# Kernel tuning notes

Measured on AMD Instinct MI355X. Metric: run time of the kernel, lower is better.

The kernel has to match this reference:

```python
import jax, jax.numpy as jnp
import numpy as np

ALPHA = 1.0
BLOCK = 128  # row block size for the pairwise L1 reduction


def _pairwise_score(features, a):
    # score[i, j] = sum_k |f[i,k] - f[j,k]| * a[k]
    # computed in row blocks to avoid the O(n^2*d) broadcast intermediate
    n, d = features.shape
    av = a[:, 0]  # [d]
    fb = features.reshape(n // BLOCK, BLOCK, d)

    def blk(fblk):  # fblk: [B, d]
        diff = jnp.abs(fblk[:, None, :] - features[None, :, :])  # [B, n, d]
        return jnp.einsum('bnd,d->bn', diff, av)                  # [B, n]

    return jax.lax.map(blk, fb).reshape(n, n)


def setup_inputs() -> dict:
    key = jax.random.key(0)
    n, d = 8192, 256
    features = jax.random.normal(key, (n, d), dtype=jnp.float32)
    a = jnp.full((d, 1), 0.01, dtype=jnp.float32)  # nn.init.constant_(a, 0.01)
    return {"features": features, "a": a}


def reference(features, a):
    score = _pairwise_score(features, a)                 # [n, n]
    adjacency = jnp.exp(-ALPHA * jax.nn.relu(score))     # [n, n]
    # D^{-1/2} A D^{-1/2} via row/col elementwise scaling (== diag mm mm)
    dsq = jnp.sum(adjacency, axis=1) ** -0.5             # [n]
    normalized = dsq[:, None] * adjacency * dsq[None, :]
    return (normalized, adjacency)
```

## Files before the change

### kernel.cpp

```cpp
#include <hip/hip_runtime.h>
#include <math.h>

#define BM 128
#define BN 128
#define BK 32

typedef unsigned int uint;

__device__ __forceinline__ uint fenc(float f) {
    uint u = __float_as_uint(f);
    return (u & 0x80000000u) ? ~u : (u | 0x80000000u);
}
__device__ __forceinline__ float fdec(uint u) {
    uint v = (u & 0x80000000u) ? (u & 0x7FFFFFFFu) : ~u;
    return __uint_as_float(v);
}

__global__ __launch_bounds__(256) void init_kernel(uint* __restrict__ flags,
                                                   float* __restrict__ rowsum,
                                                   const float* __restrict__ A,
                                                   int n, int d, int zb)
{
    const int b = blockIdx.x, t = threadIdx.x;
    if (b < zb) { int i = b * 256 + t; if (i < n) rowsum[i] = 0.f; return; }
    if (t == 0) { flags[0] = 0u; flags[1] = 0xFFFFFFFFu; flags[2] = 0u; }
    __syncthreads();
    for (int k = t; k < d; k += 256)
        if (A[k] < 0.f) atomicOr(&flags[0], 1u);
}

__global__ __launch_bounds__(256) void minmax_kernel(const float* __restrict__ F,
                                                     const float* __restrict__ A,
                                                     uint* __restrict__ flags,
                                                     int n, int d)
{
    const int total4 = n * d / 4;
    float lmin = 3.4e38f, lmax = -3.4e38f;
    for (int e4 = blockIdx.x * 256 + threadIdx.x; e4 < total4; e4 += gridDim.x * 256) {
        int e = e4 * 4;
        int dk = e % d;
        float4 f = *(const float4*)(F + e);
        float4 a = *(const float4*)(A + dk);
        float g0 = fabsf(a.x) * f.x, g1 = fabsf(a.y) * f.y;
        float g2 = fabsf(a.z) * f.z, g3 = fabsf(a.w) * f.w;
        lmin = fminf(lmin, fminf(fminf(g0, g1), fminf(g2, g3)));
        lmax = fmaxf(lmax, fmaxf(fmaxf(g0, g1), fmaxf(g2, g3)));
    }
    #pragma unroll
    for (int m = 1; m < 64; m <<= 1) {
        lmin = fminf(lmin, __shfl_xor(lmin, m));
        lmax = fmaxf(lmax, __shfl_xor(lmax, m));
    }
    if ((threadIdx.x & 63) == 0) {
        atomicMin(&flags[1], fenc(lmin));
        atomicMax(&flags[2], fenc(lmax));
    }
}

__global__ __launch_bounds__(256) void quant_kernel(const float* __restrict__ F,
                                                    const float* __restrict__ A,
                                                    const uint* __restrict__ flags,
                                                    uint* __restrict__ Q,
                                                    int n, int d)
{
    const int t = threadIdx.x;
    const int r = blockIdx.x * 32 + (t & 31);
    const int kqb = t >> 5;
    const int d4 = d >> 2;
    const float gmin = fdec(flags[1]), gmax = fdec(flags[2]);
    const float span = gmax - gmin;
    const float inv = span > 0.f ? 255.f / span : 0.f;
    for (int kq = kqb; kq < d4; kq += 8) {
        float4 f = *(const float4*)(F + (size_t)r * d + kq * 4);
        float4 a = *(const float4*)(A + kq * 4);
        uint q0 = 0, q1 = 0, q2 = 0, q3 = 0;
        if (a.x > 0.f) q0 = (uint)fminf(fmaxf((a.x * f.x - gmin) * inv + 0.5f, 0.f), 255.f);
        if (a.y > 0.f) q1 = (uint)fminf(fmaxf((a.y * f.y - gmin) * inv + 0.5f, 0.f), 255.f);
        if (a.z > 0.f) q2 = (uint)fminf(fmaxf((a.z * f.z - gmin) * inv + 0.5f, 0.f), 255.f);
        if (a.w > 0.f) q3 = (uint)fminf(fmaxf((a.w * f.w - gmin) * inv + 0.5f, 0.f), 255.f);
        Q[(size_t)kq * n + r] = q0 | (q1 << 8) | (q2 << 16) | (q3 << 24);
    }
}

__global__ __launch_bounds__(256, 3) void adj_sad_kernel(const uint* __restrict__ Q,
                                                         const uint* __restrict__ flags,
                                                         float* __restrict__ adj,
                                                         float* __restrict__ rowsum,
                                                         int n, int d)
{
    if (flags[0] != 0u) return;

    __shared__ uint As[16][128];
    __shared__ uint Bs[16][128];

    int b = blockIdx.x;
    int bx = (int)((sqrtf(8.f * (float)b + 1.f) - 1.f) * 0.5f);
    while ((bx + 1) * (bx + 2) / 2 <= b) ++bx;
    while (bx * (bx + 1) / 2 > b) --bx;
    const int by = b - bx * (bx + 1) / 2;

    const int t = threadIdx.x, tx = t & 15, ty = t >> 4;
    const int i0 = by * 128;
    const int j0 = bx * 128;
    const bool diag = (bx == by);
    const int d4 = d >> 2, chunks = d4 >> 4;

    const float gmin = fdec(flags[1]), gmax = fdec(flags[2]);
    const float step = (gmax - gmin) * (1.f / 255.f);

    uint acc[8][8] = {};

    const int kk0 = t >> 5;
    const int col = 4 * (t & 31);

    uint4 sa[2], sb[2];
    #pragma unroll
    for (int j = 0; j < 2; ++j) {
        size_t g = ((size_t)(kk0 + 8 * j)) * n;
        sa[j] = *(const uint4*)(Q + g + i0 + col);
        sb[j] = *(const uint4*)(Q + g + j0 + col);
    }

    for (int c = 0; c < chunks; ++c) {
        ((uint4*)&As[0][0])[t]       = sa[0];
        ((uint4*)&As[0][0])[256 + t] = sa[1];
        ((uint4*)&Bs[0][0])[t]       = sb[0];
        ((uint4*)&Bs[0][0])[256 + t] = sb[1];
        __syncthreads();

        if (c + 1 < chunks) {
            #pragma unroll
            for (int j = 0; j < 2; ++j) {
                size_t g = ((size_t)((c + 1) * 16 + kk0 + 8 * j)) * n;
                sa[j] = *(const uint4*)(Q + g + i0 + col);
                sb[j] = *(const uint4*)(Q + g + j0 + col);
            }
        }

        #pragma unroll
        for (int kk = 0; kk < 16; ++kk) {
            uint ar[8], br[8];
            *(uint4*)&ar[0] = *(const uint4*)&As[kk][4 * ty];
            *(uint4*)&ar[4] = *(const uint4*)&As[kk][64 + 4 * ty];
            *(uint4*)&br[0] = *(const uint4*)&Bs[kk][4 * tx];
            *(uint4*)&br[4] = *(const uint4*)&Bs[kk][64 + 4 * tx];
            #pragma unroll
            for (int m = 0; m < 8; ++m)
                #pragma unroll
                for (int cc = 0; cc < 8; ++cc)
                    acc[m][cc] = __builtin_amdgcn_sad_u8(ar[m], br[cc], acc[m][cc]);
        }
        __syncthreads();
    }

    float e[8][8];
    #pragma unroll
    for (int m = 0; m < 8; ++m)
        #pragma unroll
        for (int cc = 0; cc < 8; ++cc)
            e[m][cc] = __expf(-step * (float)acc[m][cc]);

    #pragma unroll
    for (int m = 0; m < 8; ++m) {
        const int row = i0 + (m >> 2) * 64 + 4 * ty + (m & 3);
        float rs = 0.f;
        #pragma unroll
        for (int qh = 0; qh < 2; ++qh) {
            float4 v = make_float4(e[m][qh * 4 + 0], e[m][qh * 4 + 1],
                                   e[m][qh * 4 + 2], e[m][qh * 4 + 3]);
            rs += (v.x + v.y) + (v.z + v.w);
            *(float4*)(adj + (size_t)row * n + j0 + qh * 64 + 4 * tx) = v;
        }
        rs += __shfl_xor(rs, 1);
        rs += __shfl_xor(rs, 2);
        rs += __shfl_xor(rs, 4);
        rs += __shfl_xor(rs, 8);
        if (tx == 0) atomicAdd(rowsum + row, rs);
    }

    if (!diag) {
        #pragma unroll
        for (int h = 0; h < 2; ++h)
            #pragma unroll
            for (int qh = 0; qh < 2; ++qh)
                #pragma unroll
                for (int cc = 0; cc < 4; ++cc) {
                    float4 v = make_float4(e[4 * h + 0][qh * 4 + cc],
                                           e[4 * h + 1][qh * 4 + cc],
                                           e[4 * h + 2][qh * 4 + cc],
                                           e[4 * h + 3][qh * 4 + cc]);
                    const int r = j0 + qh * 64 + 4 * tx + cc;
                    *(float4*)(adj + (size_t)r * n + i0 + 64 * h + 4 * ty) = v;
                }

        float cs[8];
        #pragma unroll
        for (int cc = 0; cc < 8; ++cc) {
            float s = 0.f;
            #pragma unroll
            for (int m = 0; m < 8; ++m) s += e[m][cc];
            s += __shfl_xor(s, 16);
            s += __shfl_xor(s, 32);
            cs[cc] = s;
        }
        if ((t & 48) == 0) {
            #pragma unroll
            for (int qh = 0; qh < 2; ++qh)
                #pragma unroll
                for (int cc = 0; cc < 4; ++cc)
                    atomicAdd(rowsum + j0 + qh * 64 + 4 * tx + cc, cs[qh * 4 + cc]);
        }
    }
}

__global__ __launch_bounds__(256) void adj_kernel(
    const float* __restrict__ F, const float* __restrict__ A,
    const uint* __restrict__ flags,
    float* __restrict__ adj, float* __restrict__ rowsum, int n, int d)
{
    if (flags[0] == 0u) return;

    __shared__ __align__(16) float As[BK][BM + 4];
    __shared__ __align__(16) float Bs[BK][BN + 4];
    __shared__ float aw[256];

    const int t  = threadIdx.x;
    const int tx = t & 15;
    const int ty = t >> 4;
    const int i0 = blockIdx.y * BM;
    const int j0 = blockIdx.x * BN;

    for (int k = t; k < d; k += 256) aw[k] = A[k];

    float acc[2][2][4][4] = {};

    const int lr = t >> 3;
    const int lk = (t & 7) << 2;

    for (int kc = 0; kc < d; kc += BK) {
        __syncthreads();
        #pragma unroll
        for (int s = 0; s < 4; ++s) {
            int r = lr + 32 * s;
            float4 v = *(const float4*)(F + (size_t)(i0 + r) * d + kc + lk);
            As[lk + 0][r] = v.x; As[lk + 1][r] = v.y;
            As[lk + 2][r] = v.z; As[lk + 3][r] = v.w;
            float4 u = *(const float4*)(F + (size_t)(j0 + r) * d + kc + lk);
            Bs[lk + 0][r] = u.x; Bs[lk + 1][r] = u.y;
            Bs[lk + 2][r] = u.z; Bs[lk + 3][r] = u.w;
        }
        __syncthreads();

        #pragma unroll
        for (int k = 0; k < BK; ++k) {
            float av[2][4], bv[2][4];
            *(float4*)&av[0][0] = *(const float4*)&As[k][4 * ty];
            *(float4*)&av[1][0] = *(const float4*)&As[k][64 + 4 * ty];
            *(float4*)&bv[0][0] = *(const float4*)&Bs[k][4 * tx];
            *(float4*)&bv[1][0] = *(const float4*)&Bs[k][64 + 4 * tx];
            const float w = aw[kc + k];
            #pragma unroll
            for (int p = 0; p < 2; ++p)
                #pragma unroll
                for (int m = 0; m < 4; ++m)
                    #pragma unroll
                    for (int q = 0; q < 2; ++q)
                        #pragma unroll
                        for (int c = 0; c < 4; ++c)
                            acc[p][q][m][c] += fabsf(av[p][m] - bv[q][c]) * w;
        }
    }

    #pragma unroll
    for (int p = 0; p < 2; ++p) {
        #pragma unroll
        for (int m = 0; m < 4; ++m) {
            const int row = i0 + p * 64 + ty * 4 + m;
            float rs = 0.f;
            #pragma unroll
            for (int q = 0; q < 2; ++q) {
                float4 v;
                v.x = __expf(-fmaxf(acc[p][q][m][0], 0.f));
                v.y = __expf(-fmaxf(acc[p][q][m][1], 0.f));
                v.z = __expf(-fmaxf(acc[p][q][m][2], 0.f));
                v.w = __expf(-fmaxf(acc[p][q][m][3], 0.f));
                rs += (v.x + v.y) + (v.z + v.w);
                *(float4*)(adj + (size_t)row * n + j0 + q * 64 + tx * 4) = v;
            }
            rs += __shfl_xor(rs, 1);
            rs += __shfl_xor(rs, 2);
            rs += __shfl_xor(rs, 4);
            rs += __shfl_xor(rs, 8);
            if (tx == 0) atomicAdd(rowsum + row, rs);
        }
    }
}

__global__ __launch_bounds__(256) void dsq_kernel(
    const float* __restrict__ rowsum, float* __restrict__ dsq, int n)
{
    int i = blockIdx.x * 256 + threadIdx.x;
    if (i < n) dsq[i] = 1.f / sqrtf(rowsum[i]);
}

__global__ __launch_bounds__(256) void norm_kernel(
    const float* __restrict__ adj, const float* __restrict__ dsq,
    float* __restrict__ out, int n)
{
    const int i = blockIdx.y;
    const float di = dsq[i];
    const int base = blockIdx.x * 4096;
    #pragma unroll
    for (int k = 0; k < 4; ++k) {
        const int j = base + k * 1024 + threadIdx.x * 4;
        if (j >= n) return;
        float4 a = *(const float4*)(adj + (size_t)i * n + j);
        float4 dj = *(const float4*)(dsq + j);
        float4 o;
        o.x = di * a.x * dj.x;
        o.y = di * a.y * dj.y;
        o.z = di * a.z * dj.z;
        o.w = di * a.w * dj.w;
        *(float4*)(out + (size_t)i * n + j) = o;
    }
}

extern "C" void kernel_launch(void* const* d_in, const int* in_sizes, int n_in,
                              void* d_out, int out_size, void* d_ws, size_t ws_size,
                              hipStream_t stream)
{
    const float* F = (const float*)d_in[0];
    const float* A = (const float*)d_in[1];
    const int d = in_sizes[1];
    const int n = in_sizes[0] / d;

    float* out    = (float*)d_out;
    float* adj    = out + (size_t)n * n;
    uint*  flags  = (uint*)d_ws;
    float* rowsum = (float*)d_ws + 8;
    float* dsq    = rowsum + n;
    uint* Q = (uint*)d_out;

    const int zb = (n + 255) / 256;
    init_kernel<<<dim3(zb + 1), dim3(256), 0, stream>>>(flags, rowsum, A, n, d, zb);
    minmax_kernel<<<dim3(256), dim3(256), 0, stream>>>(F, A, flags, n, d);
    quant_kernel<<<dim3(n / 32), dim3(256), 0, stream>>>(F, A, flags, Q, n, d);

    const int nb = n / 128;
    const int tri = nb * (nb + 1) / 2;
    adj_sad_kernel<<<dim3(tri), dim3(256), 0, stream>>>(Q, flags, adj, rowsum, n, d);
    adj_kernel<<<dim3(nb, nb), dim3(256), 0, stream>>>(F, A, flags, adj, rowsum, n, d);

    dsq_kernel<<<dim3((n + 255) / 256), dim3(256), 0, stream>>>(rowsum, dsq, n);

    dim3 gridN((n + 4095) / 4096, n);
    norm_kernel<<<gridN, dim3(256), 0, stream>>>(adj, dsq, out, n);
}
```

Before: 323.6 us.

## Recompute SAD tile in second pass to fuse normalization and skip adj reload

When the workspace can hold the quantized features, the first SAD pass only accumulates row sums and skips writing the adjacency. A second SAD pass then recomputes the tile and writes both adjacency and the normalized output directly, using nontemporal stores. This removes the full n×n adjacency write-then-read round trip of the separate normalization kernel. The cost is a second pass of SAD compute. The fp32 fallback and norm kernels become grid-stride loops with fixed grid sizes.

Measured after the change: 341.4 us. 1.06x slower.

```diff
diff --git a/kernel.cpp b/kernel.cpp
--- a/kernel.cpp
+++ b/kernel.cpp
@@ -1,11 +1,8 @@
 #include <hip/hip_runtime.h>
 #include <math.h>
 
-#define BM 128
-#define BN 128
-#define BK 32
-
 typedef unsigned int uint;
+typedef float f32x4 __attribute__((ext_vector_type(4)));
 
 __device__ __forceinline__ uint fenc(float f) {
     uint u = __float_as_uint(f);
@@ -14,6 +11,11 @@
 __device__ __forceinline__ float fdec(uint u) {
     uint v = (u & 0x80000000u) ? (u & 0x7FFFFFFFu) : ~u;
     return __uint_as_float(v);
+}
+
+__device__ __forceinline__ void ntst(float* p, float a, float b, float c, float d) {
+    f32x4 t; t.x = a; t.y = b; t.z = c; t.w = d;
+    __builtin_nontemporal_store(t, (f32x4*)p);
 }
 
 __global__ __launch_bounds__(256) void init_kernel(uint* __restrict__ flags,
@@ -82,34 +84,12 @@
     }
 }
 
-__global__ __launch_bounds__(256, 3) void adj_sad_kernel(const uint* __restrict__ Q,
-                                                         const uint* __restrict__ flags,
-                                                         float* __restrict__ adj,
-                                                         float* __restrict__ rowsum,
-                                                         int n, int d)
-{
-    if (flags[0] != 0u) return;
-
-    __shared__ uint As[16][128];
-    __shared__ uint Bs[16][128];
-
-    int b = blockIdx.x;
-    int bx = (int)((sqrtf(8.f * (float)b + 1.f) - 1.f) * 0.5f);
-    while ((bx + 1) * (bx + 2) / 2 <= b) ++bx;
-    while (bx * (bx + 1) / 2 > b) --bx;
-    const int by = b - bx * (bx + 1) / 2;
-
-    const int t = threadIdx.x, tx = t & 15, ty = t >> 4;
-    const int i0 = by * 128;
-    const int j0 = bx * 128;
-    const bool diag = (bx == by);
-    const int d4 = d >> 2, chunks = d4 >> 4;
-
-    const float gmin = fdec(flags[1]), gmax = fdec(flags[2]);
-    const float step = (gmax - gmin) * (1.f / 255.f);
-
-    uint acc[8][8] = {};
-
+__device__ __forceinline__ void sad_core(const uint* __restrict__ Q, int n, int chunks,
+                                         int i0, int j0, int t,
+                                         uint (&acc)[8][8],
+                                         uint (&As)[16][128], uint (&Bs)[16][128])
+{
+    const int tx = t & 15, ty = t >> 4;
     const int kk0 = t >> 5;
     const int col = 4 * (t & 31);
 
@@ -152,13 +132,42 @@
         }
         __syncthreads();
     }
-
-    float e[8][8];
+}
+
+__device__ __forceinline__ void tri_decode(int b, int& bx, int& by) {
+    bx = (int)((sqrtf(8.f * (float)b + 1.f) - 1.f) * 0.5f);
+    while ((bx + 1) * (bx + 2) / 2 <= b) ++bx;
+    while (bx * (bx + 1) / 2 > b) --bx;
+    by = b - bx * (bx + 1) / 2;
+}
+
+__global__ __launch_bounds__(256, 3) void pass1_sad(const uint* __restrict__ Q,
+                                                    const uint* __restrict__ flags,
+                                                    float* __restrict__ adj,
+                                                    float* __restrict__ rowsum,
+                                                    int n, int d, int writeAdj)
+{
+    if (flags[0] != 0u) return;
+
+    __shared__ uint As[16][128];
+    __shared__ uint Bs[16][128];
+
+    int bx, by; tri_decode(blockIdx.x, bx, by);
+    const int t = threadIdx.x, tx = t & 15, ty = t >> 4;
+    const int i0 = by * 128, j0 = bx * 128;
+    const bool diag = (bx == by);
+
+    const float gmin = fdec(flags[1]), gmax = fdec(flags[2]);
+    const float step = (gmax - gmin) * (1.f / 255.f);
+
+    uint acc[8][8] = {};
+    sad_core(Q, n, (d >> 2) >> 4, i0, j0, t, acc, As, Bs);
+
     #pragma unroll
     for (int m = 0; m < 8; ++m)
         #pragma unroll
         for (int cc = 0; cc < 8; ++cc)
-            e[m][cc] = __expf(-step * (float)acc[m][cc]);
+            acc[m][cc] = __float_as_uint(__expf(-step * (float)acc[m][cc]));
 
     #pragma unroll
     for (int m = 0; m < 8; ++m) {
@@ -166,10 +175,13 @@
         float rs = 0.f;
         #pragma unroll
         for (int qh = 0; qh < 2; ++qh) {
-            float4 v = make_float4(e[m][qh * 4 + 0], e[m][qh * 4 + 1],
-                                   e[m][qh * 4 + 2], e[m][qh * 4 + 3]);
+            float4 v = make_float4(__uint_as_float(acc[m][qh * 4 + 0]),
+                                   __uint_as_float(acc[m][qh * 4 + 1]),
+                                   __uint_as_float(acc[m][qh * 4 + 2]),
+                                   __uint_as_float(acc[m][qh * 4 + 3]));
             rs += (v.x + v.y) + (v.z + v.w);
-            *(float4*)(adj + (size_t)row * n + j0 + qh * 64 + 4 * tx) = v;
+            if (writeAdj)
+                *(float4*)(adj + (size_t)row * n + j0 + qh * 64 + 4 * tx) = v;
         }
         rs += __shfl_xor(rs, 1);
         rs += __shfl_xor(rs, 2);
@@ -179,26 +191,27 @@
     }
 
     if (!diag) {
-        #pragma unroll
-        for (int h = 0; h < 2; ++h)
-            #pragma unroll
-            for (int qh = 0; qh < 2; ++qh)
-                #pragma unroll
-                for (int cc = 0; cc < 4; ++cc) {
-                    float4 v = make_float4(e[4 * h + 0][qh * 4 + cc],
-                                           e[4 * h + 1][qh * 4 + cc],
-                                           e[4 * h + 2][qh * 4 + cc],
-                                           e[4 * h + 3][qh * 4 + cc]);
-                    const int r = j0 + qh * 64 + 4 * tx + cc;
-                    *(float4*)(adj + (size_t)r * n + i0 + 64 * h + 4 * ty) = v;
-                }
-
+        if (writeAdj) {
+            #pragma unroll
+            for (int h = 0; h < 2; ++h)
+                #pragma unroll
+                for (int qh = 0; qh < 2; ++qh)
+                    #pragma unroll
+                    for (int cc = 0; cc < 4; ++cc) {
+                        float4 v = make_float4(__uint_as_float(acc[4 * h + 0][qh * 4 + cc]),
+                                               __uint_as_float(acc[4 * h + 1][qh * 4 + cc]),
+                                               __uint_as_float(acc[4 * h + 2][qh * 4 + cc]),
+                                               __uint_as_float(acc[4 * h + 3][qh * 4 + cc]));
+                        const int r = j0 + qh * 64 + 4 * tx + cc;
+                        *(float4*)(adj + (size_t)r * n + i0 + 64 * h + 4 * ty) = v;
+                    }
+        }
         float cs[8];
         #pragma unroll
         for (int cc = 0; cc < 8; ++cc) {
             float s = 0.f;
             #pragma unroll
-            for (int m = 0; m < 8; ++m) s += e[m][cc];
+            for (int m = 0; m < 8; ++m) s += __uint_as_float(acc[m][cc]);
             s += __shfl_xor(s, 16);
             s += __shfl_xor(s, 32);
             cs[cc] = s;
@@ -213,86 +226,165 @@
     }
 }
 
-__global__ __launch_bounds__(256) void adj_kernel(
+__global__ __launch_bounds__(256, 3) void pass2_sad(const uint* __restrict__ Q,
+                                                    const uint* __restrict__ flags,
+                                                    const float* __restrict__ dsq,
+                                                    float* __restrict__ adj,
+                                                    float* __restrict__ nrm,
+                                                    int n, int d)
+{
+    if (flags[0] != 0u) return;
+
+    __shared__ uint As[16][128];
+    __shared__ uint Bs[16][128];
+
+    int bx, by; tri_decode(blockIdx.x, bx, by);
+    const int t = threadIdx.x, tx = t & 15, ty = t >> 4;
+    const int i0 = by * 128, j0 = bx * 128;
+    const bool diag = (bx == by);
+
+    const float gmin = fdec(flags[1]), gmax = fdec(flags[2]);
+    const float step = (gmax - gmin) * (1.f / 255.f);
+
+    uint acc[8][8] = {};
+    sad_core(Q, n, (d >> 2) >> 4, i0, j0, t, acc, As, Bs);
+
+    #pragma unroll
+    for (int m = 0; m < 8; ++m)
+        #pragma unroll
+        for (int cc = 0; cc < 8; ++cc)
+            acc[m][cc] = __float_as_uint(__expf(-step * (float)acc[m][cc]));
+
+    float dr[8], dc[8];
+    #pragma unroll
+    for (int m = 0; m < 8; ++m)
+        dr[m] = dsq[i0 + (m >> 2) * 64 + 4 * ty + (m & 3)];
+    *(float4*)&dc[0] = *(const float4*)(dsq + j0 + 4 * tx);
+    *(float4*)&dc[4] = *(const float4*)(dsq + j0 + 64 + 4 * tx);
+
+    #pragma unroll
+    for (int m = 0; m < 8; ++m) {
+        const int row = i0 + (m >> 2) * 64 + 4 * ty + (m & 3);
+        #pragma unroll
+        for (int qh = 0; qh < 2; ++qh) {
+            float e0 = __uint_as_float(acc[m][qh * 4 + 0]);
+            float e1 = __uint_as_float(acc[m][qh * 4 + 1]);
+            float e2 = __uint_as_float(acc[m][qh * 4 + 2]);
+            float e3 = __uint_as_float(acc[m][qh * 4 + 3]);
+            float* ap = adj + (size_t)row * n + j0 + qh * 64 + 4 * tx;
+            float* np = nrm + (size_t)row * n + j0 + qh * 64 + 4 * tx;
+            ntst(ap, e0, e1, e2, e3);
+            ntst(np, e0 * dr[m] * dc[qh * 4 + 0], e1 * dr[m] * dc[qh * 4 + 1],
+                     e2 * dr[m] * dc[qh * 4 + 2], e3 * dr[m] * dc[qh * 4 + 3]);
+        }
+    }
+
+    if (!diag) {
+        #pragma unroll
+        for (int h = 0; h < 2; ++h)
+            #pragma unroll
+            for (int qh = 0; qh < 2; ++qh)
+                #pragma unroll
+                for (int cc = 0; cc < 4; ++cc) {
+                    float e0 = __uint_as_float(acc[4 * h + 0][qh * 4 + cc]);
+                    float e1 = __uint_as_float(acc[4 * h + 1][qh * 4 + cc]);
+                    float e2 = __uint_as_float(acc[4 * h + 2][qh * 4 + cc]);
+                    float e3 = __uint_as_float(acc[4 * h + 3][qh * 4 + cc]);
+                    const int r = j0 + qh * 64 + 4 * tx + cc;
+                    const float dcv = dc[qh * 4 + cc];
+                    float* ap = adj + (size_t)r * n + i0 + 64 * h + 4 * ty;
+                    float* np = nrm + (size_t)r * n + i0 + 64 * h + 4 * ty;
+                    ntst(ap, e0, e1, e2, e3);
+                    ntst(np, e0 * dr[4 * h + 0] * dcv, e1 * dr[4 * h + 1] * dcv,
+                             e2 * dr[4 * h + 2] * dcv, e3 * dr[4 * h + 3] * dcv);
+                }
+    }
+}
+
+__global__ __launch_bounds__(256) void adj_fp32_kernel(
     const float* __restrict__ F, const float* __restrict__ A,
     const uint* __restrict__ flags,
     float* __restrict__ adj, float* __restrict__ rowsum, int n, int d)
 {
     if (flags[0] == 0u) return;
 
-    __shared__ __align__(16) float As[BK][BM + 4];
-    __shared__ __align__(16) float Bs[BK][BN + 4];
+    __shared__ __align__(16) float As[32][132];
+    __shared__ __align__(16) float Bs[32][132];
     __shared__ float aw[256];
 
     const int t  = threadIdx.x;
     const int tx = t & 15;
     const int ty = t >> 4;
-    const int i0 = blockIdx.y * BM;
-    const int j0 = blockIdx.x * BN;
+    const int nb = n / 128;
 
     for (int k = t; k < d; k += 256) aw[k] = A[k];
 
-    float acc[2][2][4][4] = {};
-
-    const int lr = t >> 3;
-    const int lk = (t & 7) << 2;
-
-    for (int kc = 0; kc < d; kc += BK) {
+    for (int bt = blockIdx.x; bt < nb * nb; bt += gridDim.x) {
+        const int i0 = (bt / nb) * 128;
+        const int j0 = (bt % nb) * 128;
+
+        float acc[2][2][4][4] = {};
+        const int lr = t >> 3;
+        const int lk = (t & 7) << 2;
+
+        for (int kc = 0; kc < d; kc += 32) {
+            __syncthreads();
+            #pragma unroll
+            for (int s = 0; s < 4; ++s) {
+                int r = lr + 32 * s;
+                float4 v = *(const float4*)(F + (size_t)(i0 + r) * d + kc + lk);
+                As[lk + 0][r] = v.x; As[lk + 1][r] = v.y;
+                As[lk + 2][r] = v.z; As[lk + 3][r] = v.w;
+                float4 u = *(const float4*)(F + (size_t)(j0 + r) * d + kc + lk);
+                Bs[lk + 0][r] = u.x; Bs[lk + 1][r] = u.y;
+                Bs[lk + 2][r] = u.z; Bs[lk + 3][r] = u.w;
+            }
+            __syncthreads();
+
+            #pragma unroll
+            for (int k = 0; k < 32; ++k) {
+                float av[2][4], bv[2][4];
+                *(float4*)&av[0][0] = *(const float4*)&As[k][4 * ty];
+                *(float4*)&av[1][0] = *(const float4*)&As[k][64 + 4 * ty];
+                *(float4*)&bv[0][0] = *(const float4*)&Bs[k][4 * tx];
+                *(float4*)&bv[1][0] = *(const float4*)&Bs[k][64 + 4 * tx];
+                const float w = aw[kc + k];
+                #pragma unroll
+                for (int p = 0; p < 2; ++p)
+                    #pragma unroll
+                    for (int m = 0; m < 4; ++m)
+                        #pragma unroll
+                        for (int q = 0; q < 2; ++q)
+                            #pragma unroll
+                            for (int c = 0; c < 4; ++c)
+                                acc[p][q][m][c] += fabsf(av[p][m] - bv[q][c]) * w;
+            }
+        }
+
+        #pragma unroll
+        for (int p = 0; p < 2; ++p) {
+            #pragma unroll
+            for (int m = 0; m < 4; ++m) {
+                const int row = i0 + p * 64 + ty * 4 + m;
+                float rs = 0.f;
+                #pragma unroll
+                for (int q = 0; q < 2; ++q) {
+                    float4 v;
+                    v.x = __expf(-fmaxf(acc[p][q][m][0], 0.f));
+                    v.y = __expf(-fmaxf(acc[p][q][m][1], 0.f));
+                    v.z = __expf(-fmaxf(acc[p][q][m][2], 0.f));
+                    v.w = __expf(-fmaxf(acc[p][q][m][3], 0.f));
+                    rs += (v.x + v.y) + (v.z + v.w);
+                    *(float4*)(adj + (size_t)row * n + j0 + q * 64 + tx * 4) = v;
+                }
+                rs += __shfl_xor(rs, 1);
+                rs += __shfl_xor(rs, 2);
+                rs += __shfl_xor(rs, 4);
+                rs += __shfl_xor(rs, 8);
+                if (tx == 0) atomicAdd(rowsum + row, rs);
+            }
+        }
         __syncthreads();
-        #pragma unroll
-        for (int s = 0; s < 4; ++s) {
-            int r = lr + 32 * s;
-            float4 v = *(const float4*)(F + (size_t)(i0 + r) * d + kc + lk);
-            As[lk + 0][r] = v.x; As[lk + 1][r] = v.y;
-            As[lk + 2][r] = v.z; As[lk + 3][r] = v.w;
-            float4 u = *(const float4*)(F + (size_t)(j0 + r) * d + kc + lk);
-            Bs[lk + 0][r] = u.x; Bs[lk + 1][r] = u.y;
-            Bs[lk + 2][r] = u.z; Bs[lk + 3][r] = u.w;
-        }
-        __syncthreads();
-
-        #pragma unroll
-        for (int k = 0; k < BK; ++k) {
-            float av[2][4], bv[2][4];
-            *(float4*)&av[0][0] = *(const float4*)&As[k][4 * ty];
-            *(float4*)&av[1][0] = *(const float4*)&As[k][64 + 4 * ty];
-            *(float4*)&bv[0][0] = *(const float4*)&Bs[k][4 * tx];
-            *(float4*)&bv[1][0] = *(const float4*)&Bs[k][64 + 4 * tx];
-            const float w = aw[kc + k];
-            #pragma unroll
-            for (int p = 0; p < 2; ++p)
-                #pragma unroll
-                for (int m = 0; m < 4; ++m)
-                    #pragma unroll
-                    for (int q = 0; q < 2; ++q)
-                        #pragma unroll
-                        for (int c = 0; c < 4; ++c)
-                            acc[p][q][m][c] += fabsf(av[p][m] - bv[q][c]) * w;
-        }
-    }
-
-    #pragma unroll
-    for (int p = 0; p < 2; ++p) {
-        #pragma unroll
-        for (int m = 0; m < 4; ++m) {
-            const int row = i0 + p * 64 + ty * 4 + m;
-            float rs = 0.f;
-            #pragma unroll
-            for (int q = 0; q < 2; ++q) {
-                float4 v;
-                v.x = __expf(-fmaxf(acc[p][q][m][0], 0.f));
-                v.y = __expf(-fmaxf(acc[p][q][m][1], 0.f));
-                v.z = __expf(-fmaxf(acc[p][q][m][2], 0.f));
-                v.w = __expf(-fmaxf(acc[p][q][m][3], 0.f));
-                rs += (v.x + v.y) + (v.z + v.w);
-                *(float4*)(adj + (size_t)row * n + j0 + q * 64 + tx * 4) = v;
-            }
-            rs += __shfl_xor(rs, 1);
-            rs += __shfl_xor(rs, 2);
-            rs += __shfl_xor(rs, 4);
-            rs += __shfl_xor(rs, 8);
-            if (tx == 0) atomicAdd(rowsum + row, rs);
-        }
     }
 }
 
@@ -305,23 +397,18 @@
 
 __global__ __launch_bounds__(256) void norm_kernel(
     const float* __restrict__ adj, const float* __restrict__ dsq,
-    float* __restrict__ out, int n)
-{
-    const int i = blockIdx.y;
-    const float di = dsq[i];
-    const int base = blockIdx.x * 4096;
-    #pragma unroll
-    for (int k = 0; k < 4; ++k) {
-        const int j = base + k * 1024 + threadIdx.x * 4;
-        if (j >= n) return;
-        float4 a = *(const float4*)(adj + (size_t)i * n + j);
-        float4 dj = *(const float4*)(dsq + j);
-        float4 o;
-        o.x = di * a.x * dj.x;
-        o.y = di * a.y * dj.y;
-        o.z = di * a.z * dj.z;
-        o.w = di * a.w * dj.w;
-        *(float4*)(out + (size_t)i * n + j) = o;
+    const uint* __restrict__ flags, float* __restrict__ out, int n, int gateNonzero)
+{
+    if (gateNonzero && flags[0] == 0u) return;
+    for (int row = blockIdx.x; row < n; row += gridDim.x) {
+        const float di = dsq[row];
+        for (int j = threadIdx.x * 4; j < n; j += 1024) {
+            float4 a = *(const float4*)(adj + (size_t)row * n + j);
+            float4 dj = *(const float4*)(dsq + j);
+            float4 o = make_float4(di * a.x * dj.x, di * a.y * dj.y,
+                                   di * a.z * dj.z, di * a.w * dj.w);
+            *(float4*)(out + (size_t)row * n + j) = o;
+        }
     }
 }
 
@@ -334,12 +421,16 @@
     const int d = in_sizes[1];
     const int n = in_sizes[0] / d;
 
-    float* out    = (float*)d_out;
-    float* adj    = out + (size_t)n * n;
+    float* nrm    = (float*)d_out;
+    float* adj    = nrm + (size_t)n * n;
     uint*  flags  = (uint*)d_ws;
     float* rowsum = (float*)d_ws + 8;
     float* dsq    = rowsum + n;
-    uint* Q = (uint*)d_out;
+
+    const size_t wsHead = ((8 + 2 * (size_t)n) * 4 + 255) & ~(size_t)255;
+    const size_t qBytes = (size_t)n * d;
+    const bool fused = (ws_size >= wsHead + qBytes);
+    uint* Q = fused ? (uint*)((char*)d_ws + wsHead) : (uint*)d_out;
 
     const int zb = (n + 255) / 256;
     init_kernel<<<dim3(zb + 1), dim3(256), 0, stream>>>(flags, rowsum, A, n, d, zb);
@@ -348,11 +439,17 @@
 
     const int nb = n / 128;
     const int tri = nb * (nb + 1) / 2;
-    adj_sad_kernel<<<dim3(tri), dim3(256), 0, stream>>>(Q, flags, adj, rowsum, n, d);
-    adj_kernel<<<dim3(nb, nb), dim3(256), 0, stream>>>(F, A, flags, adj, rowsum, n, d);
+
+    pass1_sad<<<dim3(tri), dim3(256), 0, stream>>>(Q, flags, adj, rowsum, n, d,
+                                                   fused ? 0 : 1);
+    adj_fp32_kernel<<<dim3(1024), dim3(256), 0, stream>>>(F, A, flags, adj, rowsum, n, d);
 
     dsq_kernel<<<dim3((n + 255) / 256), dim3(256), 0, stream>>>(rowsum, dsq, n);
 
-    dim3 gridN((n + 4095) / 4096, n);
-    norm_kernel<<<gridN, dim3(256), 0, stream>>>(adj, dsq, out, n);
-}
+    if (fused) {
+        pass2_sad<<<dim3(tri), dim3(256), 0, stream>>>(Q, flags, dsq, adj, nrm, n, d);
+        norm_kernel<<<dim3(1024), dim3(256), 0, stream>>>(adj, dsq, flags, nrm, n, 1);
+    } else {
+        norm_kernel<<<dim3(2048), dim3(256), 0, stream>>>(adj, dsq, flags, nrm, n, 0);
+    }
+}
```
